# Optimization experiments

Hardware: AMD Instinct MI355X
Metric: run time of the kernel (lower is better)

The kernel has to match this reference:

```python
import jax, jax.numpy as jnp
import numpy as np

POS_DIM = 3
LATENT = 128
HEADS = 4
HEAD_DIM = LATENT // HEADS
KERNEL_IN = 4 * POS_DIM - POS_DIM + 1  # q_pos,o_pos,rel,dist -> 10
N_Q = 1024
N_O = 2048
LN_EPS = 1e-5


def setup_inputs() -> dict:
    key = jax.random.key(0)
    ks = jax.random.split(key, 9)
    s = lambda fan_in: 1.0 / np.sqrt(fan_in)
    return {
        "h_obs": jax.random.normal(ks[0], (N_O, LATENT), dtype=jnp.float32),
        "pos_obs": jax.random.normal(ks[1], (N_O, POS_DIM), dtype=jnp.float32),
        "pos_query": jax.random.normal(ks[2], (N_Q, POS_DIM), dtype=jnp.float32),
        "obs_batch": jnp.zeros((N_O,), dtype=jnp.int32),
        "query_batch": jnp.zeros((N_Q,), dtype=jnp.int32),
        # kernel_mlp: Linear(10, 128) -> ReLU -> Linear(128, 4); stored as [in, out]
        "W1": jax.random.uniform(ks[3], (KERNEL_IN, LATENT), jnp.float32, -s(KERNEL_IN), s(KERNEL_IN)),
        "b1": jnp.zeros((LATENT,), jnp.float32),
        "W2": jax.random.uniform(ks[4], (LATENT, HEADS), jnp.float32, -s(LATENT), s(LATENT)),
        "b2": jnp.zeros((HEADS,), jnp.float32),
        "ln_gamma": jnp.ones((LATENT,), jnp.float32),
        "ln_beta": jnp.zeros((LATENT,), jnp.float32),
        "Wv": jax.random.uniform(ks[5], (LATENT, LATENT), jnp.float32, -s(LATENT), s(LATENT)),
        "bv": jnp.zeros((LATENT,), jnp.float32),
    }


def reference(h_obs, pos_obs, pos_query, obs_batch, query_batch,
              W1, b1, W2, b2, ln_gamma, ln_beta, Wv, bv):
    N_q, N_o = pos_query.shape[0], pos_obs.shape[0]
    # pairwise relative position encodings: [N_q, N_o, 10]
    rel = pos_query[:, None, :] - pos_obs[None, :, :]            # [N_q, N_o, P]
    dist = jnp.linalg.norm(rel, axis=-1, keepdims=True)          # [N_q, N_o, 1]
    pos_q_exp = jnp.broadcast_to(pos_query[:, None, :], rel.shape)
    pos_o_exp = jnp.broadcast_to(pos_obs[None, :, :], rel.shape)
    kernel_input = jnp.concatenate([pos_q_exp, pos_o_exp, rel, dist], axis=-1)
    # per-pair MLP score -> logits [N_q, N_o, H]
    hidden = jax.nn.relu(jnp.einsum('qok,kl->qol', kernel_input, W1) + b1)
    logits = jnp.einsum('qol,lh->qoh', hidden, W2) + b2
    # same-graph mask (softmax over N_o axis)
    batch_mask = query_batch[:, None] == obs_batch[None, :]      # [N_q, N_o]
    logits = jnp.where(batch_mask[:, :, None], logits, -jnp.inf)
    weights = jax.nn.softmax(logits, axis=1)                     # over N_o
    # value path: LayerNorm -> value_proj -> heads
    mu = jnp.mean(h_obs, axis=-1, keepdims=True)
    var = jnp.var(h_obs, axis=-1, keepdims=True)
    h_norm = (h_obs - mu) * jax.lax.rsqrt(var + LN_EPS) * ln_gamma + ln_beta
    v = (h_norm @ Wv + bv).reshape(N_o, HEADS, HEAD_DIM)         # [N_o, H, D]
    # weighted aggregation: [N_q, H, D] -> [N_q, latent]
    h_query = jnp.einsum('qoh,ohd->qhd', weights, v)
    return h_query.reshape(N_q, LATENT)
```

## Files before the change

### kernel.cpp

```cpp
#include <hip/hip_runtime.h>

#define NQ 1024
#define NO 2048
#define LAT 128
#define CHUNK 16
#define NCHUNK (NO / CHUNK)
#define LOG2E 1.4426950408889634f
#define NEG_BIG -3.0e38f
#define PART_STRIDE 136
#define SY_MAX 20
#define LDSTRIDE 68
#define LQSTRIDE 64

__global__ __launch_bounds__(256) void gano_value(
    const float* __restrict__ ln_g,
    const float* __restrict__ ln_b,
    const float* __restrict__ Wv,
    const float* __restrict__ bv,
    float* __restrict__ h)
{
    __shared__ float hn[LAT];
    __shared__ float red[8];
    __shared__ float part[LAT];
    const int t = threadIdx.x;
    const int o = blockIdx.x;
    const int d = t & 127;
    const int kh = t >> 7;

    const float x = h[(size_t)o*LAT + d];
    float s1 = x, s2 = x*x;
#pragma unroll
    for (int off = 32; off >= 1; off >>= 1) {
        s1 += __shfl_xor(s1, off);
        s2 += __shfl_xor(s2, off);
    }
    const int w = t >> 6;
    if ((t & 63) == 0) { red[w*2] = s1; red[w*2+1] = s2; }
    __syncthreads();
    const float S1 = red[0] + red[2];
    const float S2 = red[1] + red[3];
    const float mean = S1 * (1.0f/LAT);
    const float var  = S2 * (1.0f/LAT) - mean*mean;
    const float rstd = rsqrtf(var + 1e-5f);
    if (t < LAT)
        hn[d] = (x - mean) * rstd * ln_g[d] + ln_b[d];
    __syncthreads();

    float acc = kh ? 0.f : bv[d];
    const float* wp = Wv + (size_t)(kh*64)*LAT + d;
    const float* hp = hn + kh*64;
#pragma unroll 8
    for (int kk = 0; kk < 64; ++kk)
        acc = fmaf(hp[kk], wp[(size_t)kk*LAT], acc);
    if (kh) part[d] = acc;
    __syncthreads();
    if (!kh) h[(size_t)o*LAT + d] = acc + part[d];
}

__global__ __launch_bounds__(256) void gano_main(
    const float* __restrict__ v,
    const float* __restrict__ pos_obs,
    const float* __restrict__ pos_query,
    const int* __restrict__ obs_batch,
    const int* __restrict__ query_batch,
    const float* __restrict__ W1,
    const float* __restrict__ b1,
    const float* __restrict__ W2,
    float* __restrict__ part,
    float* __restrict__ out,
    int SY)
{
    __shared__ __align__(16) float ld[32*LDSTRIDE];
    __shared__ __align__(16) float lcq[32*LQSTRIDE];
    __shared__ __align__(16) float lgt[16*4*CHUNK];
    __shared__ __align__(16) float w1d[3*LAT];
    __shared__ __align__(16) float lv[CHUNK*LAT];
    __shared__ float lpos[CHUNK*3];
    __shared__ int   lob[CHUNK];

    const int tid = threadIdx.x;
    const int i  = tid & 15;
    const int qi = tid >> 4;
    const int q  = blockIdx.x * 16 + qi;
    const int d0 = i * 8;
    const int hstar = i >> 2;
    const int bsw = (i >> 2) & 1;
    const float NINF = -__builtin_inff();

    for (int idx = tid; idx < 3*LAT; idx += 256) {
        const int a = idx >> 7, dd = idx & 127;
        w1d[idx] = W1[(3+a)*LAT + dd] - W1[(6+a)*LAT + dd];
    }
#pragma unroll
    for (int t2 = 0; t2 < 2; ++t2) {
        const int idx = tid + t2*256;
        const int row = idx >> 5;
        const int g   = idx & 31;
        const int dd  = g * 4;
        const int qq  = blockIdx.x * 16 + row;
        const float px = pos_query[qq*3+0];
        const float py = pos_query[qq*3+1];
        const float pz = pos_query[qq*3+2];
        float4 c = *(const float4*)(b1 + dd);
        const float4 wx0 = *(const float4*)(W1 + 0*LAT + dd);
        const float4 wx6 = *(const float4*)(W1 + 6*LAT + dd);
        const float4 wy0 = *(const float4*)(W1 + 1*LAT + dd);
        const float4 wy6 = *(const float4*)(W1 + 7*LAT + dd);
        const float4 wz0 = *(const float4*)(W1 + 2*LAT + dd);
        const float4 wz6 = *(const float4*)(W1 + 8*LAT + dd);
        c.x = fmaf(px, wx0.x+wx6.x, fmaf(py, wy0.x+wy6.x, fmaf(pz, wz0.x+wz6.x, c.x)));
        c.y = fmaf(px, wx0.y+wx6.y, fmaf(py, wy0.y+wy6.y, fmaf(pz, wz0.y+wz6.y, c.y)));
        c.z = fmaf(px, wx0.z+wx6.z, fmaf(py, wy0.z+wy6.z, fmaf(pz, wz0.z+wz6.z, c.z)));
        c.w = fmaf(px, wx0.w+wx6.w, fmaf(py, wy0.w+wy6.w, fmaf(pz, wz0.w+wz6.w, c.w)));
        *(float4*)(lcq + g*LQSTRIDE + row*4) = c;
    }

    const int   qb = query_batch[q];
    const float qx = pos_query[q*3+0];
    const float qy = pos_query[q*3+1];
    const float qz = pos_query[q*3+2];

    float4 accA = make_float4(0.f,0.f,0.f,0.f);
    float4 accB = make_float4(0.f,0.f,0.f,0.f);
    float m = NEG_BIG, lsum = 0.f;

    for (int cb = blockIdx.y; cb < NCHUNK; cb += SY) {
        const int o0 = cb * CHUNK;
        __syncthreads();

        for (int idx = tid; idx < CHUNK*(LAT/4); idx += 256) {
            const int oo = idx >> 5;
            const int g  = idx & 31;
            const int d4 = g * 4;
            const float* po = pos_obs + (size_t)(o0 + oo)*3;
            const float px = po[0], py = po[1], pz = po[2];
            const float4 wa = *(const float4*)(w1d + 0*LAT + d4);
            const float4 wb = *(const float4*)(w1d + 1*LAT + d4);
            const float4 wc = *(const float4*)(w1d + 2*LAT + d4);
            float4 r;
            r.x = fmaf(px, wa.x, fmaf(py, wb.x, pz*wc.x));
            r.y = fmaf(px, wa.y, fmaf(py, wb.y, pz*wc.y));
            r.z = fmaf(px, wa.z, fmaf(py, wb.z, pz*wc.z));
            r.w = fmaf(px, wa.w, fmaf(py, wb.w, pz*wc.w));
            *(float4*)(ld + g*LDSTRIDE + oo*4) = r;
            const int gs = g ^ ((g >> 3) & 1);
            *(float4*)(lv + ((idx & ~31) + gs)*4) =
                *(const float4*)(v + (size_t)o0*LAT + idx*4);
        }
        for (int idx = tid; idx < CHUNK*3; idx += 256) lpos[idx] = pos_obs[o0*3 + idx];
        for (int idx = tid; idx < CHUNK;   idx += 256) lob[idx]  = obs_batch[o0 + idx];
        __syncthreads();

        {
            const int oc = i;
            const float dx = qx - lpos[oc*3+0];
            const float dy = qy - lpos[oc*3+1];
            const float dz = qz - lpos[oc*3+2];
            const float dist = sqrtf(dx*dx + dy*dy + dz*dz);
            const int mb = (lob[oc] == qb);

            float lg0 = 0.f, lg1 = 0.f, lg2 = 0.f, lg3 = 0.f;
            const float* ldr = ld + oc*4;
            const float* lcr = lcq + qi*4;
#pragma unroll 4
            for (int j = 0; j < 32; ++j) {
                const float4 dd = *(const float4*)(ldr + j*LDSTRIDE);
                const float4 cc = *(const float4*)(lcr + j*LQSTRIDE);
                const float4 wd = *(const float4*)(W1 + 9*LAT + j*4);
                const float4 w2a = *(const float4*)(W2 + (j*4+0)*4);
                const float4 w2b = *(const float4*)(W2 + (j*4+1)*4);
                const float4 w2c = *(const float4*)(W2 + (j*4+2)*4);
                const float4 w2d = *(const float4*)(W2 + (j*4+3)*4);
                const float h0 = fmaxf(fmaf(wd.x, dist, cc.x + dd.x), 0.f);
                const float h1 = fmaxf(fmaf(wd.y, dist, cc.y + dd.y), 0.f);
                const float h2 = fmaxf(fmaf(wd.z, dist, cc.z + dd.z), 0.f);
                const float h3 = fmaxf(fmaf(wd.w, dist, cc.w + dd.w), 0.f);
                lg0 = fmaf(h0, w2a.x, lg0); lg1 = fmaf(h0, w2a.y, lg1);
                lg2 = fmaf(h0, w2a.z, lg2); lg3 = fmaf(h0, w2a.w, lg3);
                lg0 = fmaf(h1, w2b.x, lg0); lg1 = fmaf(h1, w2b.y, lg1);
                lg2 = fmaf(h1, w2b.z, lg2); lg3 = fmaf(h1, w2b.w, lg3);
                lg0 = fmaf(h2, w2c.x, lg0); lg1 = fmaf(h2, w2c.y, lg1);
                lg2 = fmaf(h2, w2c.z, lg2); lg3 = fmaf(h2, w2c.w, lg3);
                lg0 = fmaf(h3, w2d.x, lg0); lg1 = fmaf(h3, w2d.y, lg1);
                lg2 = fmaf(h3, w2d.z, lg2); lg3 = fmaf(h3, w2d.w, lg3);
            }
            const int ocr = (oc + 4*qi) & 15;
            float* lrow = lgt + (qi*4)*CHUNK + ocr;
            lrow[0*CHUNK] = mb ? lg0 * LOG2E : NINF;
            lrow[1*CHUNK] = mb ? lg1 * LOG2E : NINF;
            lrow[2*CHUNK] = mb ? lg2 * LOG2E : NINF;
            lrow[3*CHUNK] = mb ? lg3 * LOG2E : NINF;
        }
        __syncthreads();

        {
            const float* rowp = lgt + (qi*4 + hstar)*CHUNK;
            float lgv[16];
#pragma unroll
            for (int p = 0; p < 4; ++p) {
                const float4 t = *(const float4*)(rowp + ((p + qi) & 3) * 4);
                lgv[p*4+0] = t.x; lgv[p*4+1] = t.y;
                lgv[p*4+2] = t.z; lgv[p*4+3] = t.w;
            }
            const float c0 = fmaxf(fmaxf(lgv[0],lgv[1]),lgv[2]);
            const float c1 = fmaxf(fmaxf(lgv[3],lgv[4]),lgv[5]);
            const float c2 = fmaxf(fmaxf(lgv[6],lgv[7]),lgv[8]);
            const float c3 = fmaxf(fmaxf(lgv[9],lgv[10]),lgv[11]);
            const float c4 = fmaxf(fmaxf(lgv[12],lgv[13]),lgv[14]);
            const float cm = fmaxf(fmaxf(fmaxf(c0,c1),fmaxf(c2,c3)), fmaxf(c4,lgv[15]));
            const float mn = fmaxf(m, cm);
            const float alpha = exp2f(m - mn);
            m = mn;
            lsum *= alpha;
            accA.x *= alpha; accA.y *= alpha; accA.z *= alpha; accA.w *= alpha;
            accB.x *= alpha; accB.y *= alpha; accB.z *= alpha; accB.w *= alpha;
            const float* vbA = lv + (2*i + bsw)*4;
            const float* vbB = lv + (2*i + 1 - bsw)*4;
#pragma unroll 4
            for (int oc = 0; oc < CHUNK; ++oc) {
                const float p = exp2f(lgv[oc] - mn);
                const float4 vA = *(const float4*)(vbA + oc*LAT);
                const float4 vB = *(const float4*)(vbB + oc*LAT);
                lsum += p;
                accA.x = fmaf(p, vA.x, accA.x);
                accA.y = fmaf(p, vA.y, accA.y);
                accA.z = fmaf(p, vA.z, accA.z);
                accA.w = fmaf(p, vA.w, accA.w);
                accB.x = fmaf(p, vB.x, accB.x);
                accB.y = fmaf(p, vB.y, accB.y);
                accB.z = fmaf(p, vB.z, accB.z);
                accB.w = fmaf(p, vB.w, accB.w);
            }
        }
    }

    if (SY == 1) {
        const float inv = 1.0f / lsum;
        float* op = out + (size_t)q*LAT + d0;
        float4 rA, rB;
        rA.x = accA.x*inv; rA.y = accA.y*inv; rA.z = accA.z*inv; rA.w = accA.w*inv;
        rB.x = accB.x*inv; rB.y = accB.y*inv; rB.z = accB.z*inv; rB.w = accB.w*inv;
        *(float4*)op       = rA;
        *(float4*)(op + 4) = rB;
    } else {
        float* pp = part + ((size_t)blockIdx.y * NQ + q) * PART_STRIDE;
        if ((i & 3) == 0) {
            pp[hstar]     = m;
            pp[4 + hstar] = lsum;
        }
        *(float4*)(pp + 8 + d0)     = accA;
        *(float4*)(pp + 8 + d0 + 4) = accB;
    }
}

__global__ __launch_bounds__(128) void gano_combine(
    const float* __restrict__ part, float* __restrict__ out, int SY)
{
    const int q = blockIdx.x;
    const int l = threadIdx.x;
    const int h = l >> 5;
    float M = NEG_BIG, Ls = 0.f, A = 0.f;
    for (int s = 0; s < SY; ++s) {
        const float* pp = part + ((size_t)s * NQ + q) * PART_STRIDE;
        const float ms = pp[h];
        const float ls = pp[4 + h];
        const float as = pp[8 + l];
        const float Mn = fmaxf(M, ms);
        const float a0 = exp2f(M - Mn);
        const float a1 = exp2f(ms - Mn);
        Ls = Ls*a0 + ls*a1;
        A  = A *a0 + as*a1;
        M = Mn;
    }
    out[(size_t)q*LAT + l] = A / Ls;
}

extern "C" void kernel_launch(void* const* d_in, const int* in_sizes, int n_in,
                              void* d_out, int out_size, void* d_ws, size_t ws_size,
                              hipStream_t stream) {
    (void)in_sizes; (void)n_in; (void)out_size;
    float*       h_obs     = (float*)d_in[0];
    const float* pos_obs   = (const float*)d_in[1];
    const float* pos_query = (const float*)d_in[2];
    const int*   obs_batch = (const int*)d_in[3];
    const int*   query_batch = (const int*)d_in[4];
    const float* W1 = (const float*)d_in[5];
    const float* b1 = (const float*)d_in[6];
    const float* W2 = (const float*)d_in[7];
    const float* b2 = (const float*)d_in[8];
    const float* ln_g = (const float*)d_in[9];
    const float* ln_b = (const float*)d_in[10];
    const float* Wv = (const float*)d_in[11];
    const float* bv = (const float*)d_in[12];
    (void)b2;
    float* ws  = (float*)d_ws;
    float* out = (float*)d_out;

    int SY = 1;
    const size_t per = (size_t)NQ * PART_STRIDE * sizeof(float);
    if (ws && ws_size >= 2*per) {
        size_t s = ws_size / per;
        SY = (int)(s < SY_MAX ? s : SY_MAX);
    }

    gano_value<<<NO, 256, 0, stream>>>(ln_g, ln_b, Wv, bv, h_obs);
    gano_main<<<dim3(NQ/16, SY), 256, 0, stream>>>(h_obs, pos_obs, pos_query,
                                                   obs_batch, query_batch,
                                                   W1, b1, W2, ws, out, SY);
    if (SY > 1)
        gano_combine<<<NQ, 128, 0, stream>>>(ws, out, SY);
}
```

Baseline: 169.8 us.

## Compute per-pair MLP second layer with fp16 MFMA instead of scalar FMAs

The per-pair kernel MLP's second layer (128 hidden to 4 heads) moves from scalar FP32 FMAs to 16x16x32 f16 MFMA instructions. Each wave processes four queries against the 16-observation chunk, and W2 is held in register B-fragments padded to 16 columns. Query positions and batch ids are staged in shared memory, and the distance weights are moved into LDS. This aims to cut VALU work in the logit computation. In exchange, hidden activations are rounded to fp16 and 12 of the 16 MFMA output columns are wasted padding.

```diff
diff --git a/kernel.cpp b/kernel.cpp
--- a/kernel.cpp
+++ b/kernel.cpp
@@ -10,7 +10,12 @@
 #define PART_STRIDE 136
 #define SY_MAX 20
 #define LDSTRIDE 68
-#define LQSTRIDE 64
+#define LQSTRIDE 68
+
+typedef float  f32x4 __attribute__((ext_vector_type(4)));
+typedef __fp16 f16x8 __attribute__((ext_vector_type(8)));
+typedef __fp16 f16x2 __attribute__((ext_vector_type(2)));
+union afrag { f16x8 f8; f16x2 h2[4]; __fp16 h[8]; };
 
 __global__ __launch_bounds__(256) void gano_value(
     const float* __restrict__ ln_g,
@@ -73,8 +78,9 @@
     __shared__ __align__(16) float ld[32*LDSTRIDE];
     __shared__ __align__(16) float lcq[32*LQSTRIDE];
     __shared__ __align__(16) float lgt[16*4*CHUNK];
-    __shared__ __align__(16) float w1d[3*LAT];
+    __shared__ __align__(16) float w1d[4*LAT];
     __shared__ __align__(16) float lv[CHUNK*LAT];
+    __shared__ __align__(16) float lqpos[16*4];
     __shared__ float lpos[CHUNK*3];
     __shared__ int   lob[CHUNK];
 
@@ -85,11 +91,27 @@
     const int d0 = i * 8;
     const int hstar = i >> 2;
     const int bsw = (i >> 2) & 1;
+    const int lane = tid & 63;
+    const int wv2  = tid >> 6;
+    const int ocA  = lane & 15;
+    const int u    = lane >> 4;
+    const int headC = lane & 15;
     const float NINF = -__builtin_inff();
 
-    for (int idx = tid; idx < 3*LAT; idx += 256) {
+    afrag bfrag[4];
+#pragma unroll
+    for (int s = 0; s < 4; ++s)
+#pragma unroll
+        for (int e = 0; e < 8; ++e) {
+            const int kg = s*32 + u*8 + e;
+            const float wv = (headC < 4) ? W2[kg*4 + headC] : 0.f;
+            bfrag[s].h[e] = (__fp16)wv;
+        }
+
+    for (int idx = tid; idx < 4*LAT; idx += 256) {
         const int a = idx >> 7, dd = idx & 127;
-        w1d[idx] = W1[(3+a)*LAT + dd] - W1[(6+a)*LAT + dd];
+        w1d[idx] = (a < 3) ? (W1[(3+a)*LAT + dd] - W1[(6+a)*LAT + dd])
+                           : W1[9*LAT + dd];
     }
 #pragma unroll
     for (int t2 = 0; t2 < 2; ++t2) {
@@ -101,6 +123,12 @@
         const float px = pos_query[qq*3+0];
         const float py = pos_query[qq*3+1];
         const float pz = pos_query[qq*3+2];
+        if (g == 0) {
+            float4 qp;
+            qp.x = px; qp.y = py; qp.z = pz;
+            qp.w = __int_as_float(query_batch[qq]);
+            *(float4*)(lqpos + row*4) = qp;
+        }
         float4 c = *(const float4*)(b1 + dd);
         const float4 wx0 = *(const float4*)(W1 + 0*LAT + dd);
         const float4 wx6 = *(const float4*)(W1 + 6*LAT + dd);
@@ -114,11 +142,6 @@
         c.w = fmaf(px, wx0.w+wx6.w, fmaf(py, wy0.w+wy6.w, fmaf(pz, wz0.w+wz6.w, c.w)));
         *(float4*)(lcq + g*LQSTRIDE + row*4) = c;
     }
-
-    const int   qb = query_batch[q];
-    const float qx = pos_query[q*3+0];
-    const float qy = pos_query[q*3+1];
-    const float qz = pos_query[q*3+2];
 
     float4 accA = make_float4(0.f,0.f,0.f,0.f);
     float4 accB = make_float4(0.f,0.f,0.f,0.f);
@@ -151,45 +174,44 @@
         for (int idx = tid; idx < CHUNK;   idx += 256) lob[idx]  = obs_batch[o0 + idx];
         __syncthreads();
 
-        {
-            const int oc = i;
-            const float dx = qx - lpos[oc*3+0];
-            const float dy = qy - lpos[oc*3+1];
-            const float dz = qz - lpos[oc*3+2];
+#pragma unroll
+        for (int t = 0; t < 4; ++t) {
+            const int ql = 4*wv2 + t;
+            const float4 qp = *(const float4*)(lqpos + ql*4);
+            const float dx = qp.x - lpos[ocA*3+0];
+            const float dy = qp.y - lpos[ocA*3+1];
+            const float dz = qp.z - lpos[ocA*3+2];
             const float dist = sqrtf(dx*dx + dy*dy + dz*dz);
-            const int mb = (lob[oc] == qb);
-
-            float lg0 = 0.f, lg1 = 0.f, lg2 = 0.f, lg3 = 0.f;
-            const float* ldr = ld + oc*4;
-            const float* lcr = lcq + qi*4;
-#pragma unroll 4
-            for (int j = 0; j < 32; ++j) {
-                const float4 dd = *(const float4*)(ldr + j*LDSTRIDE);
-                const float4 cc = *(const float4*)(lcr + j*LQSTRIDE);
-                const float4 wd = *(const float4*)(W1 + 9*LAT + j*4);
-                const float4 w2a = *(const float4*)(W2 + (j*4+0)*4);
-                const float4 w2b = *(const float4*)(W2 + (j*4+1)*4);
-                const float4 w2c = *(const float4*)(W2 + (j*4+2)*4);
-                const float4 w2d = *(const float4*)(W2 + (j*4+3)*4);
-                const float h0 = fmaxf(fmaf(wd.x, dist, cc.x + dd.x), 0.f);
-                const float h1 = fmaxf(fmaf(wd.y, dist, cc.y + dd.y), 0.f);
-                const float h2 = fmaxf(fmaf(wd.z, dist, cc.z + dd.z), 0.f);
-                const float h3 = fmaxf(fmaf(wd.w, dist, cc.w + dd.w), 0.f);
-                lg0 = fmaf(h0, w2a.x, lg0); lg1 = fmaf(h0, w2a.y, lg1);
-                lg2 = fmaf(h0, w2a.z, lg2); lg3 = fmaf(h0, w2a.w, lg3);
-                lg0 = fmaf(h1, w2b.x, lg0); lg1 = fmaf(h1, w2b.y, lg1);
-                lg2 = fmaf(h1, w2b.z, lg2); lg3 = fmaf(h1, w2b.w, lg3);
-                lg0 = fmaf(h2, w2c.x, lg0); lg1 = fmaf(h2, w2c.y, lg1);
-                lg2 = fmaf(h2, w2c.z, lg2); lg3 = fmaf(h2, w2c.w, lg3);
-                lg0 = fmaf(h3, w2d.x, lg0); lg1 = fmaf(h3, w2d.y, lg1);
-                lg2 = fmaf(h3, w2d.z, lg2); lg3 = fmaf(h3, w2d.w, lg3);
+            const int qb = __float_as_int(qp.w);
+            f32x4 acc = {0.f, 0.f, 0.f, 0.f};
+#pragma unroll
+            for (int s = 0; s < 4; ++s) {
+                afrag a;
+#pragma unroll
+                for (int e2 = 0; e2 < 2; ++e2) {
+                    const int g = s*8 + u*2 + e2;
+                    const float4 cc = *(const float4*)(lcq + g*LQSTRIDE + ql*4);
+                    const float4 dd = *(const float4*)(ld  + g*LDSTRIDE + ocA*4);
+                    const float4 wd = *(const float4*)(w1d + 3*LAT + g*4);
+                    const float p0 = fmaxf(fmaf(dist, wd.x, cc.x + dd.x), 0.f);
+                    const float p1 = fmaxf(fmaf(dist, wd.y, cc.y + dd.y), 0.f);
+                    const float p2 = fmaxf(fmaf(dist, wd.z, cc.z + dd.z), 0.f);
+                    const float p3 = fmaxf(fmaf(dist, wd.w, cc.w + dd.w), 0.f);
+                    a.h2[e2*2+0] = __builtin_amdgcn_cvt_pkrtz(p0, p1);
+                    a.h2[e2*2+1] = __builtin_amdgcn_cvt_pkrtz(p2, p3);
+                }
+                acc = __builtin_amdgcn_mfma_f32_16x16x32_f16(a.f8, bfrag[s].f8, acc, 0, 0, 0);
             }
-            const int ocr = (oc + 4*qi) & 15;
-            float* lrow = lgt + (qi*4)*CHUNK + ocr;
-            lrow[0*CHUNK] = mb ? lg0 * LOG2E : NINF;
-            lrow[1*CHUNK] = mb ? lg1 * LOG2E : NINF;
-            lrow[2*CHUNK] = mb ? lg2 * LOG2E : NINF;
-            lrow[3*CHUNK] = mb ? lg3 * LOG2E : NINF;
+            if (headC < 4) {
+                float* lrow = lgt + (ql*4 + headC)*CHUNK;
+#pragma unroll
+                for (int r = 0; r < 4; ++r) {
+                    const int oc = u*4 + r;
+                    const int mb = (lob[oc] == qb);
+                    const int ocr = (oc + 4*ql) & 15;
+                    lrow[ocr] = mb ? acc[r] * LOG2E : NINF;
+                }
+            }
         }
         __syncthreads();
 
```

Result: slower. 181.9 us (+7.1%).
